# Performance work log

Hardware: AMD Instinct MI355X
Metric: run time of the kernel (lower is better)

The kernel has to match this reference:

```python
import jax, jax.numpy as jnp
import numpy as np
from jax import lax

DIM = 96
HEADS = 3
EPS = 1e-12


def conv1x1(x, w):
    # x: [b,c,h,w], w: [o,c]
    return jnp.einsum('bchw,oc->bohw', x, w)


def dwconv3(x, w):
    # depthwise 3x3, SAME padding. w: [C,1,3,3]
    C = x.shape[1]
    return lax.conv_general_dilated(
        x, w, window_strides=(1, 1), padding='SAME',
        feature_group_count=C,
        dimension_numbers=('NCHW', 'OIHW', 'NCHW'))


def channel_attn(q, kv, temperature):
    # q: [b,C,h,w], kv: [b,2C,h,w], temperature: [heads,1,1]
    k, v = jnp.split(kv, 2, axis=1)
    b, C, h, w = q.shape
    c = C // HEADS
    r = lambda x: x.reshape(b, HEADS, c, h * w)
    q, k, v = r(q), r(k), r(v)
    # L2-normalize along the (h*w) axis (torch F.normalize semantics)
    qn = q / jnp.maximum(jnp.linalg.norm(q, axis=-1, keepdims=True), EPS)
    kn = k / jnp.maximum(jnp.linalg.norm(k, axis=-1, keepdims=True), EPS)
    attn = jnp.einsum('bhcn,bhdn->bhcd', qn, kn) * temperature  # [b,heads,c,c]
    attn = jax.nn.softmax(attn, axis=-1)
    out = jnp.einsum('bhcd,bhdn->bhcn', attn, v)
    return out.reshape(b, C, h, w)


def setup_inputs() -> dict:
    key = jax.random.key(0)
    ks = jax.random.split(key, 16)
    d = DIM
    s = lambda fan: 1.0 / np.sqrt(fan)
    inp = {
        'low': jax.random.normal(ks[0], (2, d, 256, 256), jnp.float32),
        'high': jax.random.normal(ks[1], (2, d, 256, 256), jnp.float32),
        'temperature': jnp.ones((HEADS, 1, 1), jnp.float32),
        'qc_w': jax.random.normal(ks[2], (d, d), jnp.float32) * s(d),
        'qdw_c_w': jax.random.normal(ks[3], (d, 1, 3, 3), jnp.float32) * s(9),
        'kvc_w': jax.random.normal(ks[4], (2 * d, d), jnp.float32) * s(d),
        'kvdw_c_w': jax.random.normal(ks[5], (2 * d, 1, 3, 3), jnp.float32) * s(9),
        'qt_w': jax.random.normal(ks[6], (d, d), jnp.float32) * s(d),
        'qdw_t_w': jax.random.normal(ks[7], (d, 1, 3, 3), jnp.float32) * s(9),
        'kvt_w': jax.random.normal(ks[8], (2 * d, d), jnp.float32) * s(d),
        'kvdw_t_w': jax.random.normal(ks[9], (2 * d, 1, 3, 3), jnp.float32) * s(9),
        'po_c_w': jax.random.normal(ks[10], (d, d), jnp.float32) * s(d),
        'po_t_w': jax.random.normal(ks[11], (d, d), jnp.float32) * s(d),
        'concat_w': jax.random.normal(ks[12], (d, 2 * d), jnp.float32) * s(2 * d),
        'concat_b': jax.random.normal(ks[13], (d,), jnp.float32) * s(2 * d),
    }
    return inp


def reference(low, high, temperature, qc_w, qdw_c_w, kvc_w, kvdw_c_w,
              qt_w, qdw_t_w, kvt_w, kvdw_t_w, po_c_w, po_t_w,
              concat_w, concat_b):
    q_c = dwconv3(conv1x1(high, qc_w), qdw_c_w)
    kv_c = dwconv3(conv1x1(high, kvc_w), kvdw_c_w)
    q_t = dwconv3(conv1x1(low, qt_w), qdw_t_w)
    kv_t = dwconv3(conv1x1(low, kvt_w), kvdw_t_w)
    out_c = conv1x1(channel_attn(q_c, kv_t, temperature), po_c_w)
    out_t = conv1x1(channel_attn(q_t, kv_c, temperature), po_t_w)
    out = jnp.concatenate([out_c, out_t], axis=1)
    out = conv1x1(out, concat_w) + concat_b[None, :, None, None]
    return out
```

## Files before the change

kernel.cpp:

```cpp
#include <hip/hip_runtime.h>
#include <hip/hip_bf16.h>

#define HW 65536
#define GNS 64

typedef __attribute__((ext_vector_type(8))) short short8;
typedef __attribute__((ext_vector_type(4))) float f32x4;
union U8 { short8 s; unsigned u[4]; ushort h[8]; };

static __device__ __forceinline__ ushort f2bf(float f) {
    union { float f; unsigned u; } v; v.f = f;
    unsigned u = v.u;
    unsigned r = (u + 0x7fffu + ((u >> 16) & 1u)) >> 16;
    return (ushort)r;
}
static __device__ __forceinline__ float bf2f(ushort u) {
    union { unsigned u; float f; } v; v.u = ((unsigned)u) << 16; return v.f;
}
static __device__ __forceinline__ unsigned pk2(float a, float b) {
    __hip_bfloat162 h = __float22bfloat162_rn(make_float2(a, b));
    union { __hip_bfloat162 h; unsigned u; } c; c.h = h; return c.u;
}
static __device__ __forceinline__ f32x4 mfma16(short8 a, short8 b, f32x4 c) {
    return __builtin_amdgcn_mfma_f32_16x16x32_bf16(a, b, c, 0, 0, 0);
}

__global__ __launch_bounds__(256) void prep_kernel(
        const float* __restrict__ qc, const float* __restrict__ kvc,
        const float* __restrict__ qt, const float* __restrict__ kvt,
        const float* __restrict__ cw, const float* __restrict__ poc, const float* __restrict__ pot,
        ushort* __restrict__ Wc, ushort* __restrict__ Wt,
        float* __restrict__ W1, float* __restrict__ W2, float* __restrict__ SSQ) {
    int bx = blockIdx.x, tid = threadIdx.x;
    if (bx < 9) {
        for (int idx = bx * 256 + tid; idx < 288 * 96; idx += 9 * 256) {
            Wc[idx] = f2bf(idx < 96 * 96 ? qc[idx] : kvc[idx - 96 * 96]);
            Wt[idx] = f2bf(idx < 96 * 96 ? qt[idx] : kvt[idx - 96 * 96]);
        }
        if (bx == 0)
            for (int idx = tid; idx < 8 * 96; idx += 256) SSQ[idx] = 0.f;
    } else {
        int idx = (bx - 9) * 256 + tid;
        int sel = idx < 9216 ? 0 : 1;
        int i = sel ? idx - 9216 : idx;
        int o = i / 96, m = i % 96;
        const float* po = sel ? pot : poc;
        float acc = 0.f;
        for (int p = 0; p < 96; ++p)
            acc += cw[o * 192 + sel * 96 + p] * po[p * 96 + m];
        (sel ? W2 : W1)[i] = acc;
    }
}

__global__ __launch_bounds__(256, 2) void conv_kernel(const float* __restrict__ X,
                                                      const ushort* __restrict__ W,
                                                      ushort* __restrict__ Y) {
    __shared__ ushort xs[96][136];
    int tid = threadIdx.x;
    int n0 = blockIdx.x * 128;
    int og = blockIdx.y;
    int b = blockIdx.z;
    int wave = tid >> 6, lane = tid & 63, lr = lane & 15, lg = lane >> 4;
    const float* Xb = X + (size_t)b * 96 * HW + n0;
    #pragma unroll
    for (int i = 0; i < 12; ++i) {
        int idx = tid + i * 256;
        int ch = idx >> 5, g = idx & 31;
        float4 v = *(const float4*)(Xb + (size_t)ch * HW + 4 * g);
        unsigned* d = (unsigned*)&xs[ch][4 * g];
        d[0] = pk2(v.x, v.y);
        d[1] = pk2(v.z, v.w);
    }
    __syncthreads();
    short8 af[2][3];
    #pragma unroll
    for (int nt = 0; nt < 2; ++nt) {
        int n = wave * 32 + nt * 16 + lr;
        #pragma unroll
        for (int kk = 0; kk < 3; ++kk) {
            int kb = kk * 32 + lg * 8;
            U8 t;
            #pragma unroll
            for (int j = 0; j < 4; ++j) {
                unsigned e0 = xs[kb + 2 * j][n];
                unsigned e1 = xs[kb + 2 * j + 1][n];
                t.u[j] = e0 | (e1 << 16);
            }
            af[nt][kk] = t.s;
        }
    }
    __syncthreads();
    const ushort* Wg = W + (size_t)og * 96 * 96 + (size_t)lr * 96 + lg * 8;
    ushort* ys = &xs[0][0];
    #pragma unroll
    for (int mt = 0; mt < 6; ++mt) {
        f32x4 a0 = {0.f, 0.f, 0.f, 0.f}, a1 = {0.f, 0.f, 0.f, 0.f};
        #pragma unroll
        for (int kk = 0; kk < 3; ++kk) {
            short8 wf = *(const short8*)(Wg + (size_t)mt * 16 * 96 + kk * 32);
            a0 = mfma16(af[0][kk], wf, a0);
            a1 = mfma16(af[1][kk], wf, a1);
        }
        unsigned* d0 = (unsigned*)&ys[(mt * 16 + lr) * 136 + wave * 32 + lg * 4];
        d0[0] = pk2(a0[0], a0[1]);
        d0[1] = pk2(a0[2], a0[3]);
        unsigned* d1 = (unsigned*)&ys[(mt * 16 + lr) * 136 + wave * 32 + 16 + lg * 4];
        d1[0] = pk2(a1[0], a1[1]);
        d1[1] = pk2(a1[2], a1[3]);
    }
    __syncthreads();
    ushort* Yg = Y + (size_t)(b * 288 + og * 96) * HW + n0;
    int row0 = tid >> 4, g = tid & 15;
    #pragma unroll
    for (int p = 0; p < 6; ++p) {
        int row = p * 16 + row0;
        *(short8*)&Yg[(size_t)row * HW + 8 * g] = *(const short8*)&ys[row * 136 + 8 * g];
    }
}

__global__ __launch_bounds__(256) void dw_kernel(const ushort* __restrict__ Y,
                                                 const float* __restrict__ qdw,
                                                 const float* __restrict__ kvdw,
                                                 ushort* __restrict__ QKV,
                                                 float* __restrict__ SSQ, int is_c) {
    __shared__ ushort tile[34 * 256];
    int tid = threadIdx.x;
    int ch = blockIdx.y % 288, b = blockIdx.y / 288;
    int r0 = blockIdx.x * 32;
    const float* w = (ch < 96) ? (qdw + ch * 9) : (kvdw + (ch - 96) * 9);
    float w00 = w[0], w01 = w[1], w02 = w[2], w10 = w[3], w11 = w[4],
          w12 = w[5], w20 = w[6], w21 = w[7], w22 = w[8];
    const ushort* src = Y + (size_t)(b * 288 + ch) * HW;
    #pragma unroll
    for (int i = 0; i < 5; ++i) {
        int idx = tid + i * 256;
        if (idx < 34 * 32) {
            int row = idx >> 5, g = idx & 31;
            int gr = r0 - 1 + row;
            short8 v;
            if (gr >= 0 && gr < 256) v = *(const short8*)(src + gr * 256 + 8 * g);
            else v = (short8){0, 0, 0, 0, 0, 0, 0, 0};
            *(short8*)&tile[row * 256 + 8 * g] = v;
        }
    }
    __syncthreads();
    int wave = tid >> 6, lane = tid & 63;
    float rows[3][6];
    float ssq = 0.f;
    #define LOADROW(LROW, D)                                                 \
    {                                                                        \
        ushort4 t4 = *(const ushort4*)&tile[(LROW) * 256 + 4 * lane];        \
        float c0 = bf2f(t4.x), c1 = bf2f(t4.y), c2 = bf2f(t4.z), c3 = bf2f(t4.w); \
        float lft = __shfl(c3, lane - 1);                                    \
        float rgt = __shfl(c0, lane + 1);                                    \
        if (lane == 0) lft = 0.f;                                            \
        if (lane == 63) rgt = 0.f;                                           \
        D[0] = lft; D[1] = c0; D[2] = c1; D[3] = c2; D[4] = c3; D[5] = rgt;  \
    }
    LOADROW(wave * 8 + 0, rows[0]);
    LOADROW(wave * 8 + 1, rows[1]);
    ushort* dst = QKV + (size_t)(b * 288 + ch) * HW;
    #pragma unroll
    for (int orow = 0; orow < 8; ++orow) {
        LOADROW(wave * 8 + orow + 2, rows[(orow + 2) % 3]);
        float* ra = rows[orow % 3];
        float* rb = rows[(orow + 1) % 3];
        float* rc = rows[(orow + 2) % 3];
        float acc[4];
        #pragma unroll
        for (int j = 0; j < 4; ++j) {
            acc[j] = w00 * ra[j] + w01 * ra[j + 1] + w02 * ra[j + 2]
                   + w10 * rb[j] + w11 * rb[j + 1] + w12 * rb[j + 2]
                   + w20 * rc[j] + w21 * rc[j + 1] + w22 * rc[j + 2];
            ssq += acc[j] * acc[j];
        }
        uint2 pv;
        pv.x = pk2(acc[0], acc[1]);
        pv.y = pk2(acc[2], acc[3]);
        *(uint2*)&dst[(r0 + wave * 8 + orow) * 256 + 4 * lane] = pv;
    }
    #undef LOADROW
    if (ch < 192) {
        #pragma unroll
        for (int off = 1; off < 64; off <<= 1) ssq += __shfl_xor(ssq, off);
        if (lane == 0) {
            int t_ = ch >= 96;
            int chq = t_ ? ch - 96 : ch;
            int a_ = is_c ? t_ : (1 - t_);
            atomicAdd(&SSQ[((a_ * 2 + b) * 2 + t_) * 96 + chq], ssq);
        }
    }
}

__global__ __launch_bounds__(256) void gram_kernel(const ushort* __restrict__ QKVc,
                                                   const ushort* __restrict__ QKVt,
                                                   float* __restrict__ Gpart) {
    __shared__ ushort qs[32 * 256];
    __shared__ ushort ks2[32 * 256];
    __shared__ float Gp[4][32][32];
    int tid = threadIdx.x, wave = tid >> 6, lane = tid & 63;
    int lr = lane & 15, lg = lane >> 4;
    int code = blockIdx.y;
    int a = code / 6, b = (code % 6) / 3, h = code % 3;
    const ushort* qsrc = (a == 0) ? QKVc : QKVt;
    const ushort* ksrc = (a == 0) ? QKVt : QKVc;
    const ushort* qb = qsrc + (size_t)(b * 288 + 32 * h) * HW + blockIdx.x * 1024;
    const ushort* kb = ksrc + (size_t)(b * 288 + 96 + 32 * h) * HW + blockIdx.x * 1024;
    f32x4 acc[2][2];
    #pragma unroll
    for (int i = 0; i < 2; ++i)
        #pragma unroll
        for (int j = 0; j < 2; ++j) acc[i][j] = (f32x4){0.f, 0.f, 0.f, 0.f};
    for (int ph = 0; ph < 4; ++ph) {
        int noff = ph * 256;
        #pragma unroll
        for (int i = 0; i < 4; ++i) {
            int idx = tid + i * 256;
            int row = idx >> 5, g = idx & 31;
            int col = (g * 8) ^ ((row & 7) << 3);
            *(short8*)&qs[row * 256 + col] = *(const short8*)(qb + (size_t)row * HW + noff + 8 * g);
            *(short8*)&ks2[row * 256 + col] = *(const short8*)(kb + (size_t)row * HW + noff + 8 * g);
        }
        __syncthreads();
        #pragma unroll
        for (int j = 0; j < 2; ++j) {
            int ks_ = wave * 2 + j;
            int c0 = (ks_ * 32 + lg * 8) ^ ((lr & 7) << 3);
            short8 a0 = *(const short8*)&qs[lr * 256 + c0];
            short8 a1 = *(const short8*)&qs[(16 + lr) * 256 + c0];
            short8 b0 = *(const short8*)&ks2[lr * 256 + c0];
            short8 b1 = *(const short8*)&ks2[(16 + lr) * 256 + c0];
            acc[0][0] = mfma16(a0, b0, acc[0][0]);
            acc[0][1] = mfma16(a0, b1, acc[0][1]);
            acc[1][0] = mfma16(a1, b0, acc[1][0]);
            acc[1][1] = mfma16(a1, b1, acc[1][1]);
        }
        __syncthreads();
    }
    #pragma unroll
    for (int i = 0; i < 2; ++i)
        #pragma unroll
        for (int j = 0; j < 2; ++j)
            #pragma unroll
            for (int r = 0; r < 4; ++r)
                Gp[wave][i * 16 + lg * 4 + r][j * 16 + lr] = acc[i][j][r];
    __syncthreads();
    float* Gout = Gpart + ((size_t)code * GNS + blockIdx.x) * 1024;
    for (int idx = tid; idx < 1024; idx += 256) {
        float ssum = 0.f;
        #pragma unroll
        for (int wv = 0; wv < 4; ++wv) ssum += (&Gp[wv][0][0])[idx];
        Gout[idx] = ssum;
    }
}

__global__ __launch_bounds__(256) void attn_kernel(const float* __restrict__ Gpart,
                                                   const float* __restrict__ SSQ,
                                                   const float* __restrict__ temperature,
                                                   const float* __restrict__ W1,
                                                   const float* __restrict__ W2,
                                                   ushort* __restrict__ Mcat) {
    __shared__ float Gs[1024];
    __shared__ float nq[32], nk[32], A[32][32];
    int tid = threadIdx.x;
    int code = blockIdx.x;
    int a = code / 6, b = (code % 6) / 3, h = code % 3;
    const float* gp = Gpart + (size_t)code * GNS * 1024;
    #pragma unroll
    for (int j = 0; j < 4; ++j) {
        int idx = tid + j * 256;
        float s = 0.f;
        #pragma unroll 8
        for (int p = 0; p < GNS; ++p) s += gp[(size_t)p * 1024 + idx];
        Gs[idx] = s;
    }
    if (tid < 32)
        nq[tid] = fmaxf(sqrtf(fmaxf(SSQ[((a * 2 + b) * 2 + 0) * 96 + 32 * h + tid], 0.f)), 1e-12f);
    else if (tid < 64)
        nk[tid - 32] = fmaxf(sqrtf(fmaxf(SSQ[((a * 2 + b) * 2 + 1) * 96 + 32 * h + (tid - 32)], 0.f)), 1e-12f);
    __syncthreads();
    if (tid < 32) {
        float t = temperature[h];
        float lgv[32];
        float inq = t / nq[tid];
        float mx = -1e30f;
        #pragma unroll
        for (int j = 0; j < 32; ++j) { lgv[j] = Gs[tid * 32 + j] * inq / nk[j]; mx = fmaxf(mx, lgv[j]); }
        float ssum = 0.f;
        #pragma unroll
        for (int j = 0; j < 32; ++j) { lgv[j] = expf(lgv[j] - mx); ssum += lgv[j]; }
        float inv = 1.f / ssum;
        #pragma unroll
        for (int j = 0; j < 32; ++j) A[tid][j] = lgv[j] * inv;
    }
    __syncthreads();
    const float* Wm = (a == 0) ? W1 : W2;
    for (int idx = tid; idx < 96 * 32; idx += 256) {
        int o = idx >> 5, d = idx & 31;
        float acc = 0.f;
        #pragma unroll
        for (int i = 0; i < 32; ++i)
            acc += Wm[o * 96 + 32 * h + i] * A[i][d];
        Mcat[(size_t)(b * 96 + o) * 192 + a * 96 + 32 * h + d] = f2bf(acc);
    }
}

__global__ __launch_bounds__(256, 2) void final_kernel(const ushort* __restrict__ QKVc,
                                                       const ushort* __restrict__ QKVt,
                                                       const ushort* __restrict__ Mcat,
                                                       const float* __restrict__ bias,
                                                       float* __restrict__ out) {
    __shared__ float smem[96 * 132];
    ushort* vs = (ushort*)smem;
    int tid = threadIdx.x;
    int n0 = blockIdx.x * 128, b = blockIdx.y;
    int wave = tid >> 6, lane = tid & 63, lr = lane & 15, lg = lane >> 4;
    #pragma unroll
    for (int i = 0; i < 12; ++i) {
        int idx = tid + i * 256;
        int d = idx >> 4, g = idx & 15;
        const ushort* sp = (d < 96) ? (QKVt + (size_t)(b * 288 + 192 + d) * HW)
                                    : (QKVc + (size_t)(b * 288 + 192 + (d - 96)) * HW);
        U8 t;
        t.s = *(const short8*)(sp + n0 + 8 * g);
        unsigned* dst = (unsigned*)&vs[d * 132 + 8 * g];
        dst[0] = t.u[0]; dst[1] = t.u[1]; dst[2] = t.u[2]; dst[3] = t.u[3];
    }
    __syncthreads();
    short8 vf[2][6];
    #pragma unroll
    for (int nt = 0; nt < 2; ++nt) {
        int n = wave * 32 + nt * 16 + lr;
        #pragma unroll
        for (int kk = 0; kk < 6; ++kk) {
            int kb = kk * 32 + lg * 8;
            U8 t;
            #pragma unroll
            for (int j = 0; j < 4; ++j) {
                unsigned e0 = vs[(kb + 2 * j) * 132 + n];
                unsigned e1 = vs[(kb + 2 * j + 1) * 132 + n];
                t.u[j] = e0 | (e1 << 16);
            }
            vf[nt][kk] = t.s;
        }
    }
    __syncthreads();
    const ushort* Mb = Mcat + (size_t)b * 96 * 192;
    #pragma unroll
    for (int mt = 0; mt < 6; ++mt) {
        f32x4 a0 = {0.f, 0.f, 0.f, 0.f}, a1 = {0.f, 0.f, 0.f, 0.f};
        #pragma unroll
        for (int kk = 0; kk < 6; ++kk) {
            short8 mf = *(const short8*)&Mb[(size_t)(mt * 16 + lr) * 192 + kk * 32 + lg * 8];
            a0 = mfma16(vf[0][kk], mf, a0);
            a1 = mfma16(vf[1][kk], mf, a1);
        }
        *(float4*)&smem[(mt * 16 + lr) * 132 + wave * 32 + lg * 4] =
            make_float4(a0[0], a0[1], a0[2], a0[3]);
        *(float4*)&smem[(mt * 16 + lr) * 132 + wave * 32 + 16 + lg * 4] =
            make_float4(a1[0], a1[1], a1[2], a1[3]);
    }
    __syncthreads();
    float* outb = out + (size_t)b * 96 * HW + n0;
    int row0 = tid >> 5, q = tid & 31;
    #pragma unroll
    for (int p = 0; p < 12; ++p) {
        int row = p * 8 + row0;
        float4 v = *(const float4*)&smem[row * 132 + 4 * q];
        float bb = bias[row];
        v.x += bb; v.y += bb; v.z += bb; v.w += bb;
        *(float4*)&outb[(size_t)row * HW + 4 * q] = v;
    }
}

extern "C" void kernel_launch(void* const* d_in, const int* in_sizes, int n_in,
                              void* d_out, int out_size, void* d_ws, size_t ws_size,
                              hipStream_t stream) {
    const float* low    = (const float*)d_in[0];
    const float* high   = (const float*)d_in[1];
    const float* temp   = (const float*)d_in[2];
    const float* qc_w   = (const float*)d_in[3];
    const float* qdw_c  = (const float*)d_in[4];
    const float* kvc_w  = (const float*)d_in[5];
    const float* kvdw_c = (const float*)d_in[6];
    const float* qt_w   = (const float*)d_in[7];
    const float* qdw_t  = (const float*)d_in[8];
    const float* kvt_w  = (const float*)d_in[9];
    const float* kvdw_t = (const float*)d_in[10];
    const float* po_c   = (const float*)d_in[11];
    const float* po_t   = (const float*)d_in[12];
    const float* cw     = (const float*)d_in[13];
    const float* cb     = (const float*)d_in[14];
    float* out = (float*)d_out;

    char* ws = (char*)d_ws;
    const size_t SY = (size_t)2 * 288 * HW * 2;
    ushort* Y    = (ushort*)(ws);
    ushort* QKVc = (ushort*)(ws + SY);
    ushort* QKVt = (ushort*)(ws + 2 * SY);
    float* Gpart = (float*)ws;
    char* p = ws + 3 * SY;
    ushort* Wc = (ushort*)p; p += 288 * 96 * 2;
    ushort* Wt = (ushort*)p; p += 288 * 96 * 2;
    float* W1  = (float*)p;  p += 96 * 96 * 4;
    float* W2  = (float*)p;  p += 96 * 96 * 4;
    float* SSQ = (float*)p;  p += 8 * 96 * 4;
    ushort* Mcat = (ushort*)p; p += 2 * 96 * 192 * 2;
    if ((size_t)(p - ws) > ws_size) return;

    prep_kernel<<<81, 256, 0, stream>>>(qc_w, kvc_w, qt_w, kvt_w, cw, po_c, po_t, Wc, Wt, W1, W2, SSQ);
    conv_kernel<<<dim3(512, 3, 2), 256, 0, stream>>>(high, Wc, Y);
    dw_kernel<<<dim3(8, 576), 256, 0, stream>>>(Y, qdw_c, kvdw_c, QKVc, SSQ, 1);
    conv_kernel<<<dim3(512, 3, 2), 256, 0, stream>>>(low, Wt, Y);
    dw_kernel<<<dim3(8, 576), 256, 0, stream>>>(Y, qdw_t, kvdw_t, QKVt, SSQ, 0);
    gram_kernel<<<dim3(GNS, 12), 256, 0, stream>>>(QKVc, QKVt, Gpart);
    attn_kernel<<<12, 256, 0, stream>>>(Gpart, SSQ, temp, W1, W2, Mcat);
    final_kernel<<<dim3(512, 2), 256, 0, stream>>>(QKVc, QKVt, Mcat, cb, out);
}
```

Baseline: 244.4 us.

## Fuse depthwise conv for Q/K into gram kernel, keep separate V dwconv

The 3x3 depthwise convolution for the Q and K channels now runs inside the gram kernel, straight from the 1x1-conv output, and writes bf16 tiles to shared memory instead of round-tripping Q/K through global memory. The sum-of-squares norms are computed there too. A slimmer dw kernel produces only V, and both conv outputs are kept in separate buffers. This removes a full write and read of Q/K activations, at the cost of halo reloads per two-row block, register pressure from the 34-float row buffers, and a doubled GNS split.

New measurement: 290.3 us. 1.19x slower.

```diff
diff --git a/kernel.cpp b/kernel.cpp
--- a/kernel.cpp
+++ b/kernel.cpp
@@ -2,7 +2,7 @@
 #include <hip/hip_bf16.h>
 
 #define HW 65536
-#define GNS 64
+#define GNS 128
 
 typedef __attribute__((ext_vector_type(8))) short short8;
 typedef __attribute__((ext_vector_type(4))) float f32x4;
@@ -118,19 +118,17 @@
     }
 }
 
-__global__ __launch_bounds__(256) void dw_kernel(const ushort* __restrict__ Y,
-                                                 const float* __restrict__ qdw,
-                                                 const float* __restrict__ kvdw,
-                                                 ushort* __restrict__ QKV,
-                                                 float* __restrict__ SSQ, int is_c) {
+__global__ __launch_bounds__(256) void dwv_kernel(const ushort* __restrict__ Y,
+                                                  const float* __restrict__ kvdw,
+                                                  ushort* __restrict__ V) {
     __shared__ ushort tile[34 * 256];
     int tid = threadIdx.x;
-    int ch = blockIdx.y % 288, b = blockIdx.y / 288;
+    int cv = blockIdx.y % 96, b = blockIdx.y / 96;
     int r0 = blockIdx.x * 32;
-    const float* w = (ch < 96) ? (qdw + ch * 9) : (kvdw + (ch - 96) * 9);
+    const float* w = kvdw + (96 + cv) * 9;
     float w00 = w[0], w01 = w[1], w02 = w[2], w10 = w[3], w11 = w[4],
           w12 = w[5], w20 = w[6], w21 = w[7], w22 = w[8];
-    const ushort* src = Y + (size_t)(b * 288 + ch) * HW;
+    const ushort* src = Y + (size_t)(b * 288 + 192 + cv) * HW;
     #pragma unroll
     for (int i = 0; i < 5; ++i) {
         int idx = tid + i * 256;
@@ -146,7 +144,6 @@
     __syncthreads();
     int wave = tid >> 6, lane = tid & 63;
     float rows[3][6];
-    float ssq = 0.f;
     #define LOADROW(LROW, D)                                                 \
     {                                                                        \
         ushort4 t4 = *(const ushort4*)&tile[(LROW) * 256 + 4 * lane];        \
@@ -159,7 +156,7 @@
     }
     LOADROW(wave * 8 + 0, rows[0]);
     LOADROW(wave * 8 + 1, rows[1]);
-    ushort* dst = QKV + (size_t)(b * 288 + ch) * HW;
+    ushort* dst = V + (size_t)(b * 96 + cv) * HW;
     #pragma unroll
     for (int orow = 0; orow < 8; ++orow) {
         LOADROW(wave * 8 + orow + 2, rows[(orow + 2) % 3]);
@@ -168,74 +165,129 @@
         float* rc = rows[(orow + 2) % 3];
         float acc[4];
         #pragma unroll
-        for (int j = 0; j < 4; ++j) {
+        for (int j = 0; j < 4; ++j)
             acc[j] = w00 * ra[j] + w01 * ra[j + 1] + w02 * ra[j + 2]
                    + w10 * rb[j] + w11 * rb[j + 1] + w12 * rb[j + 2]
                    + w20 * rc[j] + w21 * rc[j + 1] + w22 * rc[j + 2];
-            ssq += acc[j] * acc[j];
-        }
         uint2 pv;
         pv.x = pk2(acc[0], acc[1]);
         pv.y = pk2(acc[2], acc[3]);
         *(uint2*)&dst[(r0 + wave * 8 + orow) * 256 + 4 * lane] = pv;
     }
     #undef LOADROW
-    if (ch < 192) {
-        #pragma unroll
-        for (int off = 1; off < 64; off <<= 1) ssq += __shfl_xor(ssq, off);
-        if (lane == 0) {
-            int t_ = ch >= 96;
-            int chq = t_ ? ch - 96 : ch;
-            int a_ = is_c ? t_ : (1 - t_);
-            atomicAdd(&SSQ[((a_ * 2 + b) * 2 + t_) * 96 + chq], ssq);
-        }
-    }
-}
-
-__global__ __launch_bounds__(256) void gram_kernel(const ushort* __restrict__ QKVc,
-                                                   const ushort* __restrict__ QKVt,
-                                                   float* __restrict__ Gpart) {
-    __shared__ ushort qs[32 * 256];
-    __shared__ ushort ks2[32 * 256];
+}
+
+__global__ __launch_bounds__(256, 2) void gram_kernel(
+        const ushort* __restrict__ Yc, const ushort* __restrict__ Yt,
+        const float* __restrict__ qdw_c, const float* __restrict__ qdw_t,
+        const float* __restrict__ kvdw_c, const float* __restrict__ kvdw_t,
+        float* __restrict__ Gpart, float* __restrict__ SSQ) {
+    __shared__ ushort qs[32 * 512];
+    __shared__ ushort kss[32 * 512];
     __shared__ float Gp[4][32][32];
+    __shared__ float wgt[2][32][9];
     int tid = threadIdx.x, wave = tid >> 6, lane = tid & 63;
     int lr = lane & 15, lg = lane >> 4;
     int code = blockIdx.y;
     int a = code / 6, b = (code % 6) / 3, h = code % 3;
-    const ushort* qsrc = (a == 0) ? QKVc : QKVt;
-    const ushort* ksrc = (a == 0) ? QKVt : QKVc;
-    const ushort* qb = qsrc + (size_t)(b * 288 + 32 * h) * HW + blockIdx.x * 1024;
-    const ushort* kb = ksrc + (size_t)(b * 288 + 96 + 32 * h) * HW + blockIdx.x * 1024;
-    f32x4 acc[2][2];
+    int r0 = blockIdx.x * 2;
+    const ushort* qsrc = a ? Yt : Yc;
+    const ushort* ksrc = a ? Yc : Yt;
+    const float* qdw = a ? qdw_t : qdw_c;
+    const float* kdw = a ? kvdw_c : kvdw_t;
+    for (int idx = tid; idx < 576; idx += 256) {
+        int sel = idx >= 288;
+        int i = sel ? idx - 288 : idx;
+        int ch = i / 9, e = i % 9;
+        wgt[sel][ch][e] = sel ? kdw[(32 * h + ch) * 9 + e] : qdw[(32 * h + ch) * 9 + e];
+    }
+    __syncthreads();
+    int seg = tid & 15, chl = tid >> 4;
+    int row = r0 + (seg >> 3), cs = (seg & 7) * 32;
+#define LOAD_ROW(R, F)                                                        \
+    {                                                                         \
+        int r_ = (R);                                                         \
+        if ((unsigned)r_ < 256u) {                                            \
+            const ushort* rp = p0 + r_ * 256 + cs;                            \
+            U8 u0, u1, u2, u3;                                                \
+            u0.s = *(const short8*)(rp);                                      \
+            u1.s = *(const short8*)(rp + 8);                                  \
+            u2.s = *(const short8*)(rp + 16);                                 \
+            u3.s = *(const short8*)(rp + 24);                                 \
+            _Pragma("unroll")                                                 \
+            for (int j_ = 0; j_ < 8; ++j_) {                                  \
+                F[1 + j_] = bf2f(u0.h[j_]);  F[9 + j_] = bf2f(u1.h[j_]);      \
+                F[17 + j_] = bf2f(u2.h[j_]); F[25 + j_] = bf2f(u3.h[j_]);     \
+            }                                                                 \
+            F[0] = cs ? bf2f(rp[-1]) : 0.f;                                   \
+            F[33] = (cs < 224) ? bf2f(rp[32]) : 0.f;                          \
+        } else {                                                              \
+            _Pragma("unroll")                                                 \
+            for (int j_ = 0; j_ < 34; ++j_) F[j_] = 0.f;                      \
+        }                                                                     \
+    }
+    for (int pass = 0; pass < 4; ++pass) {
+        int sel = pass >> 1, half = pass & 1;
+        int ch = half * 16 + chl;
+        int gch = sel ? (96 + 32 * h + ch) : (32 * h + ch);
+        const ushort* p0 = (sel ? ksrc : qsrc) + (size_t)(b * 288 + gch) * HW;
+        const float* w = wgt[sel][ch];
+        float w0 = w[0], w1 = w[1], w2 = w[2], w3 = w[3], w4 = w[4],
+              w5 = w[5], w6 = w[6], w7 = w[7], w8 = w[8];
+        float fa[34], fb[34], acc[32];
+        LOAD_ROW(row - 1, fa);
+        #pragma unroll
+        for (int j = 0; j < 32; ++j)
+            acc[j] = w0 * fa[j] + w1 * fa[j + 1] + w2 * fa[j + 2];
+        LOAD_ROW(row, fb);
+        #pragma unroll
+        for (int j = 0; j < 32; ++j)
+            acc[j] += w3 * fb[j] + w4 * fb[j + 1] + w5 * fb[j + 2];
+        LOAD_ROW(row + 1, fa);
+        #pragma unroll
+        for (int j = 0; j < 32; ++j)
+            acc[j] += w6 * fa[j] + w7 * fa[j + 1] + w8 * fa[j + 2];
+        float ssq = 0.f;
+        #pragma unroll
+        for (int j = 0; j < 32; ++j) ssq += acc[j] * acc[j];
+        ssq += __shfl_xor(ssq, 1);
+        ssq += __shfl_xor(ssq, 2);
+        ssq += __shfl_xor(ssq, 4);
+        ssq += __shfl_xor(ssq, 8);
+        if (seg == 0)
+            atomicAdd(&SSQ[((a * 2 + b) * 2 + sel) * 96 + 32 * h + ch], ssq);
+        ushort* dst = sel ? kss : qs;
+        #pragma unroll
+        for (int g4 = 0; g4 < 4; ++g4) {
+            int g = (seg >> 3) * 32 + (seg & 7) * 4 + g4;
+            int off = ch * 512 + ((g * 8) ^ ((ch & 7) << 3));
+            U8 t;
+            t.u[0] = pk2(acc[g4 * 8 + 0], acc[g4 * 8 + 1]);
+            t.u[1] = pk2(acc[g4 * 8 + 2], acc[g4 * 8 + 3]);
+            t.u[2] = pk2(acc[g4 * 8 + 4], acc[g4 * 8 + 5]);
+            t.u[3] = pk2(acc[g4 * 8 + 6], acc[g4 * 8 + 7]);
+            *(short8*)&dst[off] = t.s;
+        }
+    }
+#undef LOAD_ROW
+    __syncthreads();
+    f32x4 acc2[2][2];
     #pragma unroll
     for (int i = 0; i < 2; ++i)
         #pragma unroll
-        for (int j = 0; j < 2; ++j) acc[i][j] = (f32x4){0.f, 0.f, 0.f, 0.f};
-    for (int ph = 0; ph < 4; ++ph) {
-        int noff = ph * 256;
-        #pragma unroll
-        for (int i = 0; i < 4; ++i) {
-            int idx = tid + i * 256;
-            int row = idx >> 5, g = idx & 31;
-            int col = (g * 8) ^ ((row & 7) << 3);
-            *(short8*)&qs[row * 256 + col] = *(const short8*)(qb + (size_t)row * HW + noff + 8 * g);
-            *(short8*)&ks2[row * 256 + col] = *(const short8*)(kb + (size_t)row * HW + noff + 8 * g);
-        }
-        __syncthreads();
-        #pragma unroll
-        for (int j = 0; j < 2; ++j) {
-            int ks_ = wave * 2 + j;
-            int c0 = (ks_ * 32 + lg * 8) ^ ((lr & 7) << 3);
-            short8 a0 = *(const short8*)&qs[lr * 256 + c0];
-            short8 a1 = *(const short8*)&qs[(16 + lr) * 256 + c0];
-            short8 b0 = *(const short8*)&ks2[lr * 256 + c0];
-            short8 b1 = *(const short8*)&ks2[(16 + lr) * 256 + c0];
-            acc[0][0] = mfma16(a0, b0, acc[0][0]);
-            acc[0][1] = mfma16(a0, b1, acc[0][1]);
-            acc[1][0] = mfma16(a1, b0, acc[1][0]);
-            acc[1][1] = mfma16(a1, b1, acc[1][1]);
-        }
-        __syncthreads();
+        for (int j = 0; j < 2; ++j) acc2[i][j] = (f32x4){0.f, 0.f, 0.f, 0.f};
+    #pragma unroll
+    for (int j = 0; j < 4; ++j) {
+        int ks_ = wave * 4 + j;
+        int c0 = (ks_ * 32 + lg * 8) ^ ((lr & 7) << 3);
+        short8 a0 = *(const short8*)&qs[lr * 512 + c0];
+        short8 a1 = *(const short8*)&qs[(16 + lr) * 512 + c0];
+        short8 b0 = *(const short8*)&kss[lr * 512 + c0];
+        short8 b1 = *(const short8*)&kss[(16 + lr) * 512 + c0];
+        acc2[0][0] = mfma16(a0, b0, acc2[0][0]);
+        acc2[0][1] = mfma16(a0, b1, acc2[0][1]);
+        acc2[1][0] = mfma16(a1, b0, acc2[1][0]);
+        acc2[1][1] = mfma16(a1, b1, acc2[1][1]);
     }
     #pragma unroll
     for (int i = 0; i < 2; ++i)
@@ -243,7 +295,7 @@
         for (int j = 0; j < 2; ++j)
             #pragma unroll
             for (int r = 0; r < 4; ++r)
-                Gp[wave][i * 16 + lg * 4 + r][j * 16 + lr] = acc[i][j][r];
+                Gp[wave][i * 16 + lg * 4 + r][j * 16 + lr] = acc2[i][j][r];
     __syncthreads();
     float* Gout = Gpart + ((size_t)code * GNS + blockIdx.x) * 1024;
     for (int idx = tid; idx < 1024; idx += 256) {
@@ -305,8 +357,8 @@
     }
 }
 
-__global__ __launch_bounds__(256, 2) void final_kernel(const ushort* __restrict__ QKVc,
-                                                       const ushort* __restrict__ QKVt,
+__global__ __launch_bounds__(256, 2) void final_kernel(const ushort* __restrict__ Vc,
+                                                       const ushort* __restrict__ Vt,
                                                        const ushort* __restrict__ Mcat,
                                                        const float* __restrict__ bias,
                                                        float* __restrict__ out) {
@@ -319,8 +371,8 @@
     for (int i = 0; i < 12; ++i) {
         int idx = tid + i * 256;
         int d = idx >> 4, g = idx & 15;
-        const ushort* sp = (d < 96) ? (QKVt + (size_t)(b * 288 + 192 + d) * HW)
-                                    : (QKVc + (size_t)(b * 288 + 192 + (d - 96)) * HW);
+        const ushort* sp = (d < 96) ? (Vt + (size_t)(b * 96 + d) * HW)
+                                    : (Vc + (size_t)(b * 96 + d - 96) * HW);
         U8 t;
         t.s = *(const short8*)(sp + n0 + 8 * g);
         unsigned* dst = (unsigned*)&vs[d * 132 + 8 * g];
@@ -395,10 +447,12 @@
 
     char* ws = (char*)d_ws;
     const size_t SY = (size_t)2 * 288 * HW * 2;
-    ushort* Y    = (ushort*)(ws);
-    ushort* QKVc = (ushort*)(ws + SY);
-    ushort* QKVt = (ushort*)(ws + 2 * SY);
-    float* Gpart = (float*)ws;
+    const size_t SV = (size_t)2 * 96 * HW * 2;
+    ushort* Yc = (ushort*)(ws);
+    ushort* Yt = (ushort*)(ws + SY);
+    ushort* Vc = (ushort*)(ws + 2 * SY);
+    ushort* Vt = (ushort*)(ws + 2 * SY + SV);
+    float* Gpart = (float*)(ws + 2 * SY + 2 * SV);
     char* p = ws + 3 * SY;
     ushort* Wc = (ushort*)p; p += 288 * 96 * 2;
     ushort* Wt = (ushort*)p; p += 288 * 96 * 2;
@@ -409,11 +463,11 @@
     if ((size_t)(p - ws) > ws_size) return;
 
     prep_kernel<<<81, 256, 0, stream>>>(qc_w, kvc_w, qt_w, kvt_w, cw, po_c, po_t, Wc, Wt, W1, W2, SSQ);
-    conv_kernel<<<dim3(512, 3, 2), 256, 0, stream>>>(high, Wc, Y);
-    dw_kernel<<<dim3(8, 576), 256, 0, stream>>>(Y, qdw_c, kvdw_c, QKVc, SSQ, 1);
-    conv_kernel<<<dim3(512, 3, 2), 256, 0, stream>>>(low, Wt, Y);
-    dw_kernel<<<dim3(8, 576), 256, 0, stream>>>(Y, qdw_t, kvdw_t, QKVt, SSQ, 0);
-    gram_kernel<<<dim3(GNS, 12), 256, 0, stream>>>(QKVc, QKVt, Gpart);
+    conv_kernel<<<dim3(512, 3, 2), 256, 0, stream>>>(high, Wc, Yc);
+    conv_kernel<<<dim3(512, 3, 2), 256, 0, stream>>>(low, Wt, Yt);
+    gram_kernel<<<dim3(GNS, 12), 256, 0, stream>>>(Yc, Yt, qdw_c, qdw_t, kvdw_c, kvdw_t, Gpart, SSQ);
+    dwv_kernel<<<dim3(8, 192), 256, 0, stream>>>(Yc, kvdw_c, Vc);
+    dwv_kernel<<<dim3(8, 192), 256, 0, stream>>>(Yt, kvdw_t, Vt);
     attn_kernel<<<12, 256, 0, stream>>>(Gpart, SSQ, temp, W1, W2, Mcat);
-    final_kernel<<<dim3(512, 2), 256, 0, stream>>>(QKVc, QKVt, Mcat, cb, out);
-}
+    final_kernel<<<dim3(512, 2), 256, 0, stream>>>(Vc, Vt, Mcat, cb, out);
+}
```
